# Kernel tuning notes

Hardware: AMD Instinct MI355X
Metric: run time of the kernel (lower is better)

## Reference

```python
import jax, jax.numpy as jnp
import numpy as np

N = 100000      # nodes
E = 800000      # edges
P = 200000      # number of subgraph permutations
L = 16          # lrp_length
D = 64          # lrp_out_dim (== lrp_in_dim)
PL = P * L
LEN_SEQ = 4     # int(sqrt(L))
NUM_BOND = 4


def setup_inputs() -> dict:
    key = jax.random.key(0)
    ks = jax.random.split(key, 16)
    inp = {}
    inp["nfeat"] = jax.random.normal(ks[0], (N, D), jnp.float32)
    inp["degs"] = jax.random.uniform(ks[1], (N,), jnp.float32) * 8.0 + 1.0
    inp["n2p_val"] = jnp.ones((PL,), jnp.float32)
    inp["e2p_val"] = jnp.ones((PL,), jnp.float32)
    inp["pool_val"] = jax.random.uniform(ks[2], (P,), jnp.float32)
    inp["weights"] = jax.random.normal(ks[3], (D, D, L), jnp.float32)
    inp["bias"] = jnp.zeros((1, D), jnp.float32)
    inp["w_deg0"] = jax.random.normal(ks[4], (2 * D, LEN_SEQ), jnp.float32) * 0.3
    inp["b_deg0"] = jnp.zeros((2 * D,), jnp.float32)
    inp["w_deg1"] = jax.random.normal(ks[5], (D, 2 * D), jnp.float32) * 0.1
    inp["b_deg1"] = jnp.zeros((D,), jnp.float32)
    inp["w_lin"] = jax.random.normal(ks[6], (D, D), jnp.float32) * 0.1
    inp["b_lin"] = jnp.zeros((D,), jnp.float32)
    inp["bond_emb"] = jax.random.normal(ks[7], (NUM_BOND, D), jnp.float32)
    inp["edge_feat_idx"] = jax.random.randint(ks[8], (E,), 0, NUM_BOND, jnp.int32)
    inp["n2p_row"] = jnp.arange(PL, dtype=jnp.int32)
    inp["n2p_col"] = jax.random.randint(ks[9], (PL,), 0, N, jnp.int32)
    inp["e2p_row"] = jnp.arange(PL, dtype=jnp.int32)
    inp["e2p_col"] = jax.random.randint(ks[10], (PL,), 0, E, jnp.int32)
    inp["pool_row"] = jax.random.randint(ks[11], (P,), 0, N, jnp.int32)
    inp["pool_col"] = jnp.arange(P, dtype=jnp.int32)
    return inp


def _spmm(row, col, val, x, m):
    # COO spmm: out[r] = sum_{nnz with row==r} val * x[col]
    return jax.ops.segment_sum(val[:, None] * x[col], row, num_segments=m)


def reference(nfeat, degs, n2p_val, e2p_val, pool_val, weights, bias,
              w_deg0, b_deg0, w_deg1, b_deg1, w_lin, b_lin, bond_emb,
              edge_feat_idx, n2p_row, n2p_col, e2p_row, e2p_col,
              pool_row, pool_col):
    n = nfeat.shape[0]
    pl = n2p_row.shape[0]
    d = weights.shape[0]
    l = weights.shape[2]
    p = pl // l
    len_seq = int(round(l ** 0.5))

    efeat = bond_emb[edge_feat_idx]                                  # [E, D]
    perm = _spmm(n2p_row, n2p_col, n2p_val, nfeat, pl) \
         + _spmm(e2p_row, e2p_col, e2p_val, efeat, pl)               # [P*L, D]
    deg_perm = _spmm(n2p_row, n2p_col, n2p_val, degs[:, None], pl)   # [P*L, 1]

    x = perm.reshape(p, l, d)                                        # [P, L, D]
    deg_sel = deg_perm.reshape(p, l)[:, ::len_seq + 1]               # [P, len_seq]

    h = jnp.einsum('pab,bca->pc', x, weights) + bias                 # [P, D]
    h = jax.nn.relu(h) @ w_lin.T + b_lin                             # linear(relu(.))

    g = jax.nn.relu(deg_sel @ w_deg0.T + b_deg0) @ w_deg1.T + b_deg1  # [P, D]
    h = h * g

    out = _spmm(pool_row, pool_col, pool_val, h, n)                  # [N, D]
    return out
```

## Files before the change

kernel.cpp:

```cpp
#include <hip/hip_runtime.h>
#include <hip/hip_bf16.h>

typedef __attribute__((ext_vector_type(8))) __bf16 bf16x8;
typedef __attribute__((ext_vector_type(4))) float floatx4;
typedef __attribute__((ext_vector_type(2))) float floatx2;
typedef __attribute__((ext_vector_type(4))) int intx4;
typedef __attribute__((ext_vector_type(2))) unsigned uintx2;

constexpr int N_NODES = 100000;
constexpr int P_PERM  = 200000;

constexpr size_t W2F_OFF  = 0;
constexpr size_t WLF_OFF  = 131072;
constexpr size_t WD1F_OFF = 139264;
constexpr size_t BE_OFF   = 155648;
constexpr size_t NF8_OFF  = 3355648;
constexpr size_t WS_NEED_FULL = 3355648 + (size_t)N_NODES * 64;

__device__ inline unsigned pack_fp8x4(float x0, float x1, float x2, float x3) {
  int w = __builtin_amdgcn_cvt_pk_fp8_f32(x0, x1, 0, false);
  w = __builtin_amdgcn_cvt_pk_fp8_f32(x2, x3, w, true);
  return (unsigned)w;
}
__device__ inline floatx2 unpk_fp8_lo(unsigned w) {
  return __builtin_amdgcn_cvt_pk_f32_fp8((int)w, false);
}
__device__ inline floatx2 unpk_fp8_hi(unsigned w) {
  return __builtin_amdgcn_cvt_pk_f32_fp8((int)w, true);
}

__global__ void prep_all_kernel(const float* __restrict__ weights,
                                const float* __restrict__ w_lin,
                                const float* __restrict__ w_deg1,
                                const float* __restrict__ nfeat,
                                const int* __restrict__ e2p_col,
                                const int* __restrict__ edge_feat_idx,
                                __bf16* __restrict__ ws_bf) {
  int b = blockIdx.x;
  int t = threadIdx.x;
  if (b < 304) {
    int i = b * 256 + t;
    if (i < 65536) {
      int j = i & 7, l = (i >> 3) & 63, ct = (i >> 9) & 3, ks = (i >> 11) & 1, a = i >> 12;
      int k = ks * 32 + (l >> 4) * 8 + j;
      int c = ct * 16 + (l & 15);
      ws_bf[W2F_OFF / 2 + i] = (__bf16)weights[k * 1024 + c * 16 + a];
    } else if (i < 65536 + 4096) {
      int i2 = i - 65536;
      int j = i2 & 7, l = (i2 >> 3) & 63, ct = (i2 >> 9) & 3, ks = (i2 >> 11) & 1;
      int k = ks * 32 + (l >> 4) * 8 + j;
      int c = ct * 16 + (l & 15);
      ws_bf[WLF_OFF / 2 + i2] = (__bf16)w_lin[c * 64 + k];
    } else if (i < 65536 + 4096 + 8192) {
      int i3 = i - 65536 - 4096;
      int j = i3 & 7, l = (i3 >> 3) & 63, ct = (i3 >> 9) & 3, ks = (i3 >> 11) & 3;
      int k = ks * 32 + (l >> 4) * 8 + j;
      int c = ct * 16 + (l & 15);
      ws_bf[WD1F_OFF / 2 + i3] = (__bf16)w_deg1[c * 128 + k];
    }
  } else if (b < 3429) {
    int i = (b - 304) * 256 + t;
    if (i < N_NODES * 8) {
      float4 a = *(const float4*)(nfeat + (size_t)i * 8);
      float4 c = *(const float4*)(nfeat + (size_t)i * 8 + 4);
      uintx2 o;
      o.x = pack_fp8x4(a.x, a.y, a.z, a.w);
      o.y = pack_fp8x4(c.x, c.y, c.z, c.w);
      *(uintx2*)((char*)ws_bf + NF8_OFF + (size_t)i * 8) = o;
    }
  } else {
    int i = (b - 3429) * 256 + t;
    if (i < P_PERM * 4) {
      int4 ec = ((const int4*)e2p_col)[i];
      unsigned v = (unsigned)(edge_feat_idx[ec.x] & 0xff)
                 | ((unsigned)(edge_feat_idx[ec.y] & 0xff) << 8)
                 | ((unsigned)(edge_feat_idx[ec.z] & 0xff) << 16)
                 | ((unsigned)(edge_feat_idx[ec.w] & 0xff) << 24);
      ((unsigned*)((char*)ws_bf + BE_OFF))[i] = v;
    }
  }
}

template <bool BF16FEAT>
__global__ __launch_bounds__(256, 4) void lrp_mfma_kernel(
    const float* __restrict__ nfeat,
    const float* __restrict__ degs,
    const float* __restrict__ n2p_val,
    const float* __restrict__ e2p_val,
    const float* __restrict__ pool_val,
    const float* __restrict__ bias,
    const float* __restrict__ w_deg0,
    const float* __restrict__ b_deg0,
    const float* __restrict__ b_deg1,
    const float* __restrict__ b_lin,
    const float* __restrict__ bond_emb,
    const int* __restrict__ n2p_col,
    const int* __restrict__ pool_row,
    const __bf16* __restrict__ ws_bf,
    float* __restrict__ out) {
  __shared__ __align__(16) char shbig[18432];
  char (* const fraglds)[8192] = (char(*)[8192])shbig;
  __bf16 (* const hs)[2][16][72] = (__bf16(*)[2][16][72])shbig;
  __shared__ __align__(16) __bf16 sbond[4][72];
  __shared__ __align__(16) float swdeg0[128][4];
  __shared__ float sbd0[128];
  __shared__ float sbias[64];
  __shared__ float sblin[64];
  __shared__ float sbd1[64];

  const int t = threadIdx.x;
  const int w = t >> 6;
  const int l = t & 63;
  const int m = l & 15;
  const int q = l >> 4;
  const int pbase = blockIdx.x * 128 + w * 32;
  int pb[2]  = {pbase, pbase + 16};
  bool valid[2];
  int pbc[2];
  #pragma unroll
  for (int pt = 0; pt < 2; ++pt) {
    valid[pt] = pb[pt] < P_PERM;
    pbc[pt] = valid[pt] ? pb[pt] : (P_PERM - 16);
  }

  if (t < 256) sbond[t >> 6][t & 63] = (__bf16)bond_emb[t];
  if (t < 128) {
    *(float4*)&swdeg0[t][0] = *(const float4*)(w_deg0 + t * 4);
    sbd0[t] = b_deg0[t];
  } else if (t < 192) {
    int c = t - 128;
    sbias[c] = bias[c]; sblin[c] = b_lin[c]; sbd1[c] = b_deg1[c];
  }

  const unsigned char* __restrict__ nf8 = (const unsigned char*)ws_bf + NF8_OFF;
  const bf16x8* __restrict__ WLv  = (const bf16x8*)(ws_bf + WLF_OFF / 2);
  const bf16x8* __restrict__ WD1v = (const bf16x8*)(ws_bf + WD1F_OFF / 2);
  const unsigned* __restrict__ bep = (const unsigned*)((const char*)ws_bf + BE_OFF);
  const char* __restrict__ W2bytes = (const char*)ws_bf + W2F_OFF;

  intx4 nvx[2], evx[2], ncx[2];
  int bex[2];
  #pragma unroll
  for (int pt = 0; pt < 2; ++pt) {
    size_t rb = (size_t)pbc[pt] * 16;
    nvx[pt] = *(const intx4*)(n2p_val + rb + 4 * l);
    evx[pt] = *(const intx4*)(e2p_val + rb + 4 * l);
    ncx[pt] = *(const intx4*)(n2p_col + rb + 4 * l);
    bex[pt] = (int)bep[(size_t)pbc[pt] * 4 + l];
  }
  const int selbase = m * 16;

  auto stage = [&](int a, int buf) {
    #pragma unroll
    for (int j = 0; j < 2; ++j) {
      const char* g = W2bytes + (size_t)a * 8192 + (w * 2 + j) * 1024 + l * 16;
      char* lds = &fraglds[buf][(w * 2 + j) * 1024];
      __builtin_amdgcn_global_load_lds(
          (const __attribute__((address_space(1))) unsigned*)g,
          (__attribute__((address_space(3))) unsigned*)lds, 16, 0, 0);
    }
  };
  auto gath = [&](int nc, uintx2* g) {
    #pragma unroll
    for (int ks = 0; ks < 2; ++ks) {
      if (BF16FEAT) {
        g[ks] = *(const uintx2*)(nf8 + (size_t)nc * 64 + ks * 32 + q * 8);
      } else {
        int k0 = ks * 32 + q * 8;
        float4 n0 = *(const float4*)(nfeat + (size_t)nc * 64 + k0);
        float4 n1 = *(const float4*)(nfeat + (size_t)nc * 64 + k0 + 4);
        uintx2 o;
        o.x = pack_fp8x4(n0.x, n0.y, n0.z, n0.w);
        o.y = pack_fp8x4(n1.x, n1.y, n1.z, n1.w);
        g[ks] = o;
      }
    }
  };

  floatx4 acc[2][4] = {};
  float dsnv[2][4];
  int dsnc[2][4];
  float nv0[2], ev0[2];
  int nc0[2], be0[2];
  uintx2 g_cur[2][2], g_nxt[2][2];

  #pragma unroll
  for (int pt = 0; pt < 2; ++pt) {
    nv0[pt] = __int_as_float(__builtin_amdgcn_ds_bpermute(selbase, nvx[pt][0]));
    ev0[pt] = __int_as_float(__builtin_amdgcn_ds_bpermute(selbase, evx[pt][0]));
    nc0[pt] = __builtin_amdgcn_ds_bpermute(selbase, ncx[pt][0]);
    be0[pt] = (__builtin_amdgcn_ds_bpermute(selbase, bex[pt])) & 0xff;
    gath(nc0[pt], g_cur[pt]);
  }
  stage(0, 0);
  __syncthreads();

  #pragma unroll
  for (int a = 0; a < 16; ++a) {
    const int buf = a & 1;
    float nv1[2], ev1[2];
    int nc1[2], be1[2];
    if (a < 15) {
      const int an = a + 1;
      const int sel1 = selbase + (an >> 2) * 4;
      const int sl = an & 3;
      #pragma unroll
      for (int pt = 0; pt < 2; ++pt) {
        nv1[pt] = __int_as_float(__builtin_amdgcn_ds_bpermute(sel1, nvx[pt][sl]));
        ev1[pt] = __int_as_float(__builtin_amdgcn_ds_bpermute(sel1, evx[pt][sl]));
        nc1[pt] = __builtin_amdgcn_ds_bpermute(sel1, ncx[pt][sl]);
        be1[pt] = (__builtin_amdgcn_ds_bpermute(sel1, bex[pt]) >> (sl * 8)) & 0xff;
      }
      stage(a + 1, buf ^ 1);
      #pragma unroll
      for (int pt = 0; pt < 2; ++pt) gath(nc1[pt], g_nxt[pt]);
    }

    bf16x8 afv[2][2];
    #pragma unroll
    for (int pt = 0; pt < 2; ++pt) {
      #pragma unroll
      for (int ks = 0; ks < 2; ++ks) {
        bf16x8 eb = *(const bf16x8*)&sbond[be0[pt]][ks * 32 + q * 8];
        uintx2 gw = g_cur[pt][ks];
        floatx2 x01 = unpk_fp8_lo(gw.x);
        floatx2 x23 = unpk_fp8_hi(gw.x);
        floatx2 x45 = unpk_fp8_lo(gw.y);
        floatx2 x67 = unpk_fp8_hi(gw.y);
        float xs[8] = {x01.x, x01.y, x23.x, x23.y, x45.x, x45.y, x67.x, x67.y};
        bf16x8 af;
        #pragma unroll
        for (int j = 0; j < 8; ++j)
          af[j] = (__bf16)fmaf(nv0[pt], xs[j], ev0[pt] * (float)eb[j]);
        afv[pt][ks] = af;
      }
    }
    #pragma unroll
    for (int ks = 0; ks < 2; ++ks)
      #pragma unroll
      for (int ct = 0; ct < 4; ++ct) {
        bf16x8 frag = *(const bf16x8*)&fraglds[buf][((ks * 4 + ct) * 64 + l) * 16];
        acc[0][ct] = __builtin_amdgcn_mfma_f32_16x16x32_bf16(afv[0][ks], frag, acc[0][ct], 0, 0, 0);
        acc[1][ct] = __builtin_amdgcn_mfma_f32_16x16x32_bf16(afv[1][ks], frag, acc[1][ct], 0, 0, 0);
      }

    if (a == 0 || a == 5 || a == 10 || a == 15) {
      const int jj = a / 5;
      #pragma unroll
      for (int pt = 0; pt < 2; ++pt) {
        dsnv[pt][jj] = nv0[pt];
        dsnc[pt][jj] = nc0[pt];
      }
    }

    if (a < 15) {
      __syncthreads();
      #pragma unroll
      for (int pt = 0; pt < 2; ++pt) {
        nv0[pt] = nv1[pt]; ev0[pt] = ev1[pt]; nc0[pt] = nc1[pt]; be0[pt] = be1[pt];
        g_cur[pt][0] = g_nxt[pt][0]; g_cur[pt][1] = g_nxt[pt][1];
      }
    }
  }

  float dsreg[2][4];
  #pragma unroll
  for (int pt = 0; pt < 2; ++pt)
    #pragma unroll
    for (int jj = 0; jj < 4; ++jj)
      dsreg[pt][jj] = dsnv[pt][jj] * degs[dsnc[pt][jj]];

  __syncthreads();

  floatx4 acc2[2][4] = {};
  {
    #pragma unroll
    for (int pt = 0; pt < 2; ++pt)
      #pragma unroll
      for (int ct = 0; ct < 4; ++ct) {
        float bv = sbias[ct * 16 + m];
        #pragma unroll
        for (int rr = 0; rr < 4; ++rr)
          hs[w][pt][q * 4 + rr][ct * 16 + m] =
              (__bf16)fmaxf(acc[pt][ct][rr] + bv, 0.0f);
      }
    #pragma unroll
    for (int pt = 0; pt < 2; ++pt)
      #pragma unroll
      for (int ks = 0; ks < 2; ++ks) {
        bf16x8 af2 = *(const bf16x8*)&hs[w][pt][m][ks * 32 + q * 8];
        #pragma unroll
        for (int ct = 0; ct < 4; ++ct) {
          bf16x8 frag = WLv[(ks * 4 + ct) * 64 + l];
          acc2[pt][ct] = __builtin_amdgcn_mfma_f32_16x16x32_bf16(af2, frag, acc2[pt][ct], 0, 0, 0);
        }
      }
  }

  floatx4 gacc[2][4] = {};
  #pragma unroll
  for (int ks = 0; ks < 4; ++ks) {
    const int k0 = ks * 32 + q * 8;
    bf16x8 af[2];
    #pragma unroll
    for (int j = 0; j < 8; ++j) {
      int k = k0 + j;
      float4 wr = *(const float4*)&swdeg0[k][0];
      float bk = sbd0[k];
      #pragma unroll
      for (int pt = 0; pt < 2; ++pt) {
        float v = bk;
        v = fmaf(dsreg[pt][0], wr.x, v);
        v = fmaf(dsreg[pt][1], wr.y, v);
        v = fmaf(dsreg[pt][2], wr.z, v);
        v = fmaf(dsreg[pt][3], wr.w, v);
        af[pt][j] = (__bf16)fmaxf(v, 0.0f);
      }
    }
    #pragma unroll
    for (int ct = 0; ct < 4; ++ct) {
      bf16x8 frag = WD1v[(ks * 4 + ct) * 64 + l];
      gacc[0][ct] = __builtin_amdgcn_mfma_f32_16x16x32_bf16(af[0], frag, gacc[0][ct], 0, 0, 0);
      gacc[1][ct] = __builtin_amdgcn_mfma_f32_16x16x32_bf16(af[1], frag, gacc[1][ct], 0, 0, 0);
    }
  }

  #pragma unroll
  for (int pt = 0; pt < 2; ++pt) {
    if (!valid[pt]) continue;
    intx4   pr4 = *(const intx4*)(pool_row + pb[pt] + q * 4);
    floatx4 pv4 = *(const floatx4*)(pool_val + pb[pt] + q * 4);
    #pragma unroll
    for (int rr = 0; rr < 4; ++rr) {
      float* orow = out + (size_t)pr4[rr] * 64;
      float pv = pv4[rr];
      #pragma unroll
      for (int ct = 0; ct < 4; ++ct) {
        float h2 = (acc2[pt][ct][rr] + sblin[ct * 16 + m]) *
                   (gacc[pt][ct][rr] + sbd1[ct * 16 + m]);
        atomicAdd(orow + ct * 16 + m, pv * h2);
      }
    }
  }
}

extern "C" void kernel_launch(void* const* d_in, const int* in_sizes, int n_in,
                              void* d_out, int out_size, void* d_ws, size_t ws_size,
                              hipStream_t stream) {
  const float* nfeat    = (const float*)d_in[0];
  const float* degs     = (const float*)d_in[1];
  const float* n2p_val  = (const float*)d_in[2];
  const float* e2p_val  = (const float*)d_in[3];
  const float* pool_val = (const float*)d_in[4];
  const float* weights  = (const float*)d_in[5];
  const float* bias     = (const float*)d_in[6];
  const float* w_deg0   = (const float*)d_in[7];
  const float* b_deg0   = (const float*)d_in[8];
  const float* w_deg1   = (const float*)d_in[9];
  const float* b_deg1   = (const float*)d_in[10];
  const float* w_lin    = (const float*)d_in[11];
  const float* b_lin    = (const float*)d_in[12];
  const float* bond_emb = (const float*)d_in[13];
  const int* edge_feat_idx = (const int*)d_in[14];
  const int* n2p_col    = (const int*)d_in[16];
  const int* e2p_col    = (const int*)d_in[18];
  const int* pool_row   = (const int*)d_in[19];

  float* out = (float*)d_out;
  __bf16* ws_bf = (__bf16*)d_ws;

  hipMemsetAsync(d_out, 0, (size_t)N_NODES * 64 * sizeof(float), stream);

  prep_all_kernel<<<6554, 256, 0, stream>>>(weights, w_lin, w_deg1, nfeat,
                                            e2p_col, edge_feat_idx, ws_bf);

  int grid = (P_PERM + 127) / 128;
  if (ws_size >= WS_NEED_FULL) {
    lrp_mfma_kernel<true><<<grid, 256, 0, stream>>>(
        nfeat, degs, n2p_val, e2p_val, pool_val, bias, w_deg0, b_deg0,
        b_deg1, b_lin, bond_emb, n2p_col, pool_row, ws_bf, out);
  } else {
    lrp_mfma_kernel<false><<<grid, 256, 0, stream>>>(
        nfeat, degs, n2p_val, e2p_val, pool_val, bias, w_deg0, b_deg0,
        b_deg1, b_lin, bond_emb, n2p_col, pool_row, ws_bf, out);
  }
}
```

Baseline: 274.1 us.

## Split per-wave work to 16 permutations with 512-thread blocks

Each wave now processes one 16-permutation tile instead of two, and blocks grow to 8 waves so a block still covers 128 permutations. Weight-fragment staging and the `hs` shared buffer are redistributed across the 8 waves. This halves the per-wave register footprint to raise occupancy and hide gather latency. In exchange, each LDS weight fragment feeds only one MFMA instead of two, and block-wide barriers now span more waves. The output memset is also replaced by a simple zero-fill kernel.

```diff
diff --git a/kernel.cpp b/kernel.cpp
--- a/kernel.cpp
+++ b/kernel.cpp
@@ -27,6 +27,10 @@
 }
 __device__ inline floatx2 unpk_fp8_hi(unsigned w) {
   return __builtin_amdgcn_cvt_pk_f32_fp8((int)w, true);
+}
+
+__global__ void zero_out_kernel(float4* __restrict__ out) {
+  out[blockIdx.x * 256 + threadIdx.x] = make_float4(0.f, 0.f, 0.f, 0.f);
 }
 
 __global__ void prep_all_kernel(const float* __restrict__ weights,
@@ -82,7 +86,7 @@
 }
 
 template <bool BF16FEAT>
-__global__ __launch_bounds__(256, 4) void lrp_mfma_kernel(
+__global__ __launch_bounds__(512, 4) void lrp_mfma_kernel(
     const float* __restrict__ nfeat,
     const float* __restrict__ degs,
     const float* __restrict__ n2p_val,
@@ -100,7 +104,7 @@
     float* __restrict__ out) {
   __shared__ __align__(16) char shbig[18432];
   char (* const fraglds)[8192] = (char(*)[8192])shbig;
-  __bf16 (* const hs)[2][16][72] = (__bf16(*)[2][16][72])shbig;
+  __bf16 (* const hs)[16][72] = (__bf16(*)[16][72])shbig;
   __shared__ __align__(16) __bf16 sbond[4][72];
   __shared__ __align__(16) float swdeg0[128][4];
   __shared__ float sbd0[128];
@@ -113,15 +117,9 @@
   const int l = t & 63;
   const int m = l & 15;
   const int q = l >> 4;
-  const int pbase = blockIdx.x * 128 + w * 32;
-  int pb[2]  = {pbase, pbase + 16};
-  bool valid[2];
-  int pbc[2];
-  #pragma unroll
-  for (int pt = 0; pt < 2; ++pt) {
-    valid[pt] = pb[pt] < P_PERM;
-    pbc[pt] = valid[pt] ? pb[pt] : (P_PERM - 16);
-  }
+  const int pbase = blockIdx.x * 128 + w * 16;
+  const bool valid = pbase < P_PERM;
+  const int pbc = valid ? pbase : (P_PERM - 16);
 
   if (t < 256) sbond[t >> 6][t & 63] = (__bf16)bond_emb[t];
   if (t < 128) {
@@ -138,27 +136,23 @@
   const unsigned* __restrict__ bep = (const unsigned*)((const char*)ws_bf + BE_OFF);
   const char* __restrict__ W2bytes = (const char*)ws_bf + W2F_OFF;
 
-  intx4 nvx[2], evx[2], ncx[2];
-  int bex[2];
-  #pragma unroll
-  for (int pt = 0; pt < 2; ++pt) {
-    size_t rb = (size_t)pbc[pt] * 16;
-    nvx[pt] = *(const intx4*)(n2p_val + rb + 4 * l);
-    evx[pt] = *(const intx4*)(e2p_val + rb + 4 * l);
-    ncx[pt] = *(const intx4*)(n2p_col + rb + 4 * l);
-    bex[pt] = (int)bep[(size_t)pbc[pt] * 4 + l];
+  intx4 nvx, evx, ncx;
+  int bex;
+  {
+    size_t rb = (size_t)pbc * 16;
+    nvx = *(const intx4*)(n2p_val + rb + 4 * l);
+    evx = *(const intx4*)(e2p_val + rb + 4 * l);
+    ncx = *(const intx4*)(n2p_col + rb + 4 * l);
+    bex = (int)bep[(size_t)pbc * 4 + l];
   }
   const int selbase = m * 16;
 
   auto stage = [&](int a, int buf) {
-    #pragma unroll
-    for (int j = 0; j < 2; ++j) {
-      const char* g = W2bytes + (size_t)a * 8192 + (w * 2 + j) * 1024 + l * 16;
-      char* lds = &fraglds[buf][(w * 2 + j) * 1024];
-      __builtin_amdgcn_global_load_lds(
-          (const __attribute__((address_space(1))) unsigned*)g,
-          (__attribute__((address_space(3))) unsigned*)lds, 16, 0, 0);
-    }
+    const char* g = W2bytes + (size_t)a * 8192 + w * 1024 + l * 16;
+    char* lds = &fraglds[buf][w * 1024];
+    __builtin_amdgcn_global_load_lds(
+        (const __attribute__((address_space(1))) unsigned*)g,
+        (__attribute__((address_space(3))) unsigned*)lds, 16, 0, 0);
   };
   auto gath = [&](int nc, uintx2* g) {
     #pragma unroll
@@ -177,167 +171,137 @@
     }
   };
 
-  floatx4 acc[2][4] = {};
-  float dsnv[2][4];
-  int dsnc[2][4];
-  float nv0[2], ev0[2];
-  int nc0[2], be0[2];
-  uintx2 g_cur[2][2], g_nxt[2][2];
-
-  #pragma unroll
-  for (int pt = 0; pt < 2; ++pt) {
-    nv0[pt] = __int_as_float(__builtin_amdgcn_ds_bpermute(selbase, nvx[pt][0]));
-    ev0[pt] = __int_as_float(__builtin_amdgcn_ds_bpermute(selbase, evx[pt][0]));
-    nc0[pt] = __builtin_amdgcn_ds_bpermute(selbase, ncx[pt][0]);
-    be0[pt] = (__builtin_amdgcn_ds_bpermute(selbase, bex[pt])) & 0xff;
-    gath(nc0[pt], g_cur[pt]);
-  }
+  floatx4 acc[4] = {};
+  float dsnv[4];
+  int dsnc[4];
+  float nv0, ev0;
+  int nc0, be0;
+  uintx2 g_cur[2], g_nxt[2];
+
+  nv0 = __int_as_float(__builtin_amdgcn_ds_bpermute(selbase, nvx[0]));
+  ev0 = __int_as_float(__builtin_amdgcn_ds_bpermute(selbase, evx[0]));
+  nc0 = __builtin_amdgcn_ds_bpermute(selbase, ncx[0]);
+  be0 = (__builtin_amdgcn_ds_bpermute(selbase, bex)) & 0xff;
+  gath(nc0, g_cur);
   stage(0, 0);
   __syncthreads();
 
   #pragma unroll
   for (int a = 0; a < 16; ++a) {
     const int buf = a & 1;
-    float nv1[2], ev1[2];
-    int nc1[2], be1[2];
+    float nv1, ev1;
+    int nc1, be1;
     if (a < 15) {
       const int an = a + 1;
       const int sel1 = selbase + (an >> 2) * 4;
       const int sl = an & 3;
-      #pragma unroll
-      for (int pt = 0; pt < 2; ++pt) {
-        nv1[pt] = __int_as_float(__builtin_amdgcn_ds_bpermute(sel1, nvx[pt][sl]));
-        ev1[pt] = __int_as_float(__builtin_amdgcn_ds_bpermute(sel1, evx[pt][sl]));
-        nc1[pt] = __builtin_amdgcn_ds_bpermute(sel1, ncx[pt][sl]);
-        be1[pt] = (__builtin_amdgcn_ds_bpermute(sel1, bex[pt]) >> (sl * 8)) & 0xff;
-      }
+      nv1 = __int_as_float(__builtin_amdgcn_ds_bpermute(sel1, nvx[sl]));
+      ev1 = __int_as_float(__builtin_amdgcn_ds_bpermute(sel1, evx[sl]));
+      nc1 = __builtin_amdgcn_ds_bpermute(sel1, ncx[sl]);
+      be1 = (__builtin_amdgcn_ds_bpermute(sel1, bex) >> (sl * 8)) & 0xff;
       stage(a + 1, buf ^ 1);
-      #pragma unroll
-      for (int pt = 0; pt < 2; ++pt) gath(nc1[pt], g_nxt[pt]);
-    }
-
-    bf16x8 afv[2][2];
-    #pragma unroll
-    for (int pt = 0; pt < 2; ++pt) {
-      #pragma unroll
-      for (int ks = 0; ks < 2; ++ks) {
-        bf16x8 eb = *(const bf16x8*)&sbond[be0[pt]][ks * 32 + q * 8];
-        uintx2 gw = g_cur[pt][ks];
-        floatx2 x01 = unpk_fp8_lo(gw.x);
-        floatx2 x23 = unpk_fp8_hi(gw.x);
-        floatx2 x45 = unpk_fp8_lo(gw.y);
-        floatx2 x67 = unpk_fp8_hi(gw.y);
-        float xs[8] = {x01.x, x01.y, x23.x, x23.y, x45.x, x45.y, x67.x, x67.y};
-        bf16x8 af;
-        #pragma unroll
-        for (int j = 0; j < 8; ++j)
-          af[j] = (__bf16)fmaf(nv0[pt], xs[j], ev0[pt] * (float)eb[j]);
-        afv[pt][ks] = af;
-      }
+      gath(nc1, g_nxt);
+    }
+
+    bf16x8 afv[2];
+    #pragma unroll
+    for (int ks = 0; ks < 2; ++ks) {
+      bf16x8 eb = *(const bf16x8*)&sbond[be0][ks * 32 + q * 8];
+      uintx2 gw = g_cur[ks];
+      floatx2 x01 = unpk_fp8_lo(gw.x);
+      floatx2 x23 = unpk_fp8_hi(gw.x);
+      floatx2 x45 = unpk_fp8_lo(gw.y);
+      floatx2 x67 = unpk_fp8_hi(gw.y);
+      float xs[8] = {x01.x, x01.y, x23.x, x23.y, x45.x, x45.y, x67.x, x67.y};
+      bf16x8 af;
+      #pragma unroll
+      for (int j = 0; j < 8; ++j)
+        af[j] = (__bf16)fmaf(nv0, xs[j], ev0 * (float)eb[j]);
+      afv[ks] = af;
     }
     #pragma unroll
     for (int ks = 0; ks < 2; ++ks)
       #pragma unroll
       for (int ct = 0; ct < 4; ++ct) {
         bf16x8 frag = *(const bf16x8*)&fraglds[buf][((ks * 4 + ct) * 64 + l) * 16];
-        acc[0][ct] = __builtin_amdgcn_mfma_f32_16x16x32_bf16(afv[0][ks], frag, acc[0][ct], 0, 0, 0);
-        acc[1][ct] = __builtin_amdgcn_mfma_f32_16x16x32_bf16(afv[1][ks], frag, acc[1][ct], 0, 0, 0);
+        acc[ct] = __builtin_amdgcn_mfma_f32_16x16x32_bf16(afv[ks], frag, acc[ct], 0, 0, 0);
       }
 
     if (a == 0 || a == 5 || a == 10 || a == 15) {
       const int jj = a / 5;
-      #pragma unroll
-      for (int pt = 0; pt < 2; ++pt) {
-        dsnv[pt][jj] = nv0[pt];
-        dsnc[pt][jj] = nc0[pt];
-      }
+      dsnv[jj] = nv0;
+      dsnc[jj] = nc0;
     }
 
     if (a < 15) {
       __syncthreads();
-      #pragma unroll
-      for (int pt = 0; pt < 2; ++pt) {
-        nv0[pt] = nv1[pt]; ev0[pt] = ev1[pt]; nc0[pt] = nc1[pt]; be0[pt] = be1[pt];
-        g_cur[pt][0] = g_nxt[pt][0]; g_cur[pt][1] = g_nxt[pt][1];
+      nv0 = nv1; ev0 = ev1; nc0 = nc1; be0 = be1;
+      g_cur[0] = g_nxt[0]; g_cur[1] = g_nxt[1];
+    }
+  }
+
+  float dsreg[4];
+  #pragma unroll
+  for (int jj = 0; jj < 4; ++jj)
+    dsreg[jj] = dsnv[jj] * degs[dsnc[jj]];
+
+  __syncthreads();
+
+  floatx4 acc2[4] = {};
+  {
+    #pragma unroll
+    for (int ct = 0; ct < 4; ++ct) {
+      float bv = sbias[ct * 16 + m];
+      #pragma unroll
+      for (int rr = 0; rr < 4; ++rr)
+        hs[w][q * 4 + rr][ct * 16 + m] =
+            (__bf16)fmaxf(acc[ct][rr] + bv, 0.0f);
+    }
+    #pragma unroll
+    for (int ks = 0; ks < 2; ++ks) {
+      bf16x8 af2 = *(const bf16x8*)&hs[w][m][ks * 32 + q * 8];
+      #pragma unroll
+      for (int ct = 0; ct < 4; ++ct) {
+        bf16x8 frag = WLv[(ks * 4 + ct) * 64 + l];
+        acc2[ct] = __builtin_amdgcn_mfma_f32_16x16x32_bf16(af2, frag, acc2[ct], 0, 0, 0);
       }
     }
   }
 
-  float dsreg[2][4];
-  #pragma unroll
-  for (int pt = 0; pt < 2; ++pt)
-    #pragma unroll
-    for (int jj = 0; jj < 4; ++jj)
-      dsreg[pt][jj] = dsnv[pt][jj] * degs[dsnc[pt][jj]];
-
-  __syncthreads();
-
-  floatx4 acc2[2][4] = {};
-  {
-    #pragma unroll
-    for (int pt = 0; pt < 2; ++pt)
-      #pragma unroll
-      for (int ct = 0; ct < 4; ++ct) {
-        float bv = sbias[ct * 16 + m];
-        #pragma unroll
-        for (int rr = 0; rr < 4; ++rr)
-          hs[w][pt][q * 4 + rr][ct * 16 + m] =
-              (__bf16)fmaxf(acc[pt][ct][rr] + bv, 0.0f);
-      }
-    #pragma unroll
-    for (int pt = 0; pt < 2; ++pt)
-      #pragma unroll
-      for (int ks = 0; ks < 2; ++ks) {
-        bf16x8 af2 = *(const bf16x8*)&hs[w][pt][m][ks * 32 + q * 8];
-        #pragma unroll
-        for (int ct = 0; ct < 4; ++ct) {
-          bf16x8 frag = WLv[(ks * 4 + ct) * 64 + l];
-          acc2[pt][ct] = __builtin_amdgcn_mfma_f32_16x16x32_bf16(af2, frag, acc2[pt][ct], 0, 0, 0);
-        }
-      }
-  }
-
-  floatx4 gacc[2][4] = {};
+  floatx4 gacc[4] = {};
   #pragma unroll
   for (int ks = 0; ks < 4; ++ks) {
     const int k0 = ks * 32 + q * 8;
-    bf16x8 af[2];
+    bf16x8 af;
     #pragma unroll
     for (int j = 0; j < 8; ++j) {
       int k = k0 + j;
       float4 wr = *(const float4*)&swdeg0[k][0];
-      float bk = sbd0[k];
-      #pragma unroll
-      for (int pt = 0; pt < 2; ++pt) {
-        float v = bk;
-        v = fmaf(dsreg[pt][0], wr.x, v);
-        v = fmaf(dsreg[pt][1], wr.y, v);
-        v = fmaf(dsreg[pt][2], wr.z, v);
-        v = fmaf(dsreg[pt][3], wr.w, v);
-        af[pt][j] = (__bf16)fmaxf(v, 0.0f);
-      }
+      float v = sbd0[k];
+      v = fmaf(dsreg[0], wr.x, v);
+      v = fmaf(dsreg[1], wr.y, v);
+      v = fmaf(dsreg[2], wr.z, v);
+      v = fmaf(dsreg[3], wr.w, v);
+      af[j] = (__bf16)fmaxf(v, 0.0f);
     }
     #pragma unroll
     for (int ct = 0; ct < 4; ++ct) {
       bf16x8 frag = WD1v[(ks * 4 + ct) * 64 + l];
-      gacc[0][ct] = __builtin_amdgcn_mfma_f32_16x16x32_bf16(af[0], frag, gacc[0][ct], 0, 0, 0);
-      gacc[1][ct] = __builtin_amdgcn_mfma_f32_16x16x32_bf16(af[1], frag, gacc[1][ct], 0, 0, 0);
-    }
-  }
-
-  #pragma unroll
-  for (int pt = 0; pt < 2; ++pt) {
-    if (!valid[pt]) continue;
-    intx4   pr4 = *(const intx4*)(pool_row + pb[pt] + q * 4);
-    floatx4 pv4 = *(const floatx4*)(pool_val + pb[pt] + q * 4);
+      gacc[ct] = __builtin_amdgcn_mfma_f32_16x16x32_bf16(af, frag, gacc[ct], 0, 0, 0);
+    }
+  }
+
+  if (valid) {
+    intx4   pr4 = *(const intx4*)(pool_row + pbase + q * 4);
+    floatx4 pv4 = *(const floatx4*)(pool_val + pbase + q * 4);
     #pragma unroll
     for (int rr = 0; rr < 4; ++rr) {
       float* orow = out + (size_t)pr4[rr] * 64;
       float pv = pv4[rr];
       #pragma unroll
       for (int ct = 0; ct < 4; ++ct) {
-        float h2 = (acc2[pt][ct][rr] + sblin[ct * 16 + m]) *
-                   (gacc[pt][ct][rr] + sbd1[ct * 16 + m]);
+        float h2 = (acc2[ct][rr] + sblin[ct * 16 + m]) *
+                   (gacc[ct][rr] + sbd1[ct * 16 + m]);
         atomicAdd(orow + ct * 16 + m, pv * h2);
       }
     }
@@ -369,18 +333,17 @@
   float* out = (float*)d_out;
   __bf16* ws_bf = (__bf16*)d_ws;
 
-  hipMemsetAsync(d_out, 0, (size_t)N_NODES * 64 * sizeof(float), stream);
-
+  zero_out_kernel<<<6250, 256, 0, stream>>>((float4*)out);
   prep_all_kernel<<<6554, 256, 0, stream>>>(weights, w_lin, w_deg1, nfeat,
                                             e2p_col, edge_feat_idx, ws_bf);
 
   int grid = (P_PERM + 127) / 128;
   if (ws_size >= WS_NEED_FULL) {
-    lrp_mfma_kernel<true><<<grid, 256, 0, stream>>>(
+    lrp_mfma_kernel<true><<<grid, 512, 0, stream>>>(
         nfeat, degs, n2p_val, e2p_val, pool_val, bias, w_deg0, b_deg0,
         b_deg1, b_lin, bond_emb, n2p_col, pool_row, ws_bf, out);
   } else {
-    lrp_mfma_kernel<false><<<grid, 256, 0, stream>>>(
+    lrp_mfma_kernel<false><<<grid, 512, 0, stream>>>(
         nfeat, degs, n2p_val, e2p_val, pool_val, bias, w_deg0, b_deg0,
         b_deg1, b_lin, bond_emb, n2p_col, pool_row, ws_bf, out);
   }
```

Measured after the change: 288.4 us. 5.2% more time.
